# Kernel optimization log

Measured on AMD Instinct MI355X. Metric: run time of the kernel, lower is better.

Reference implementation:

```python
import jax, jax.numpy as jnp
import numpy as np

BS, N = 4, 4096
C_IN, C_DSSP, C_HID, NB = 384, 64, 128, 4


def setup_inputs() -> dict:
    key = jax.random.key(0)
    ks = jax.random.split(key, 12)
    sc = lambda k, sh, fan: jax.random.normal(k, sh, jnp.float32) / np.sqrt(fan)
    return {
        "s": jax.random.normal(ks[0], (BS, N, C_IN), jnp.float32),
        "s_initial": jax.random.normal(ks[1], (BS, N, C_IN), jnp.float32),
        "dssp": jax.random.normal(ks[2], (BS, N, C_DSSP), jnp.float32),
        "W_in": sc(ks[3], (C_HID, C_IN), C_IN), "b_in": jnp.zeros((C_HID,), jnp.float32),
        "W_init": sc(ks[4], (C_HID, C_IN), C_IN), "b_init": jnp.zeros((C_HID,), jnp.float32),
        "W_dssp": sc(ks[5], (C_HID, C_DSSP), C_DSSP), "b_dssp": jnp.zeros((C_HID,), jnp.float32),
        "W1": sc(ks[6], (NB, C_HID, C_HID), C_HID), "b1": jnp.zeros((NB, C_HID), jnp.float32),
        "W2": sc(ks[7], (NB, C_HID, C_HID), C_HID), "b2": jnp.zeros((NB, C_HID), jnp.float32),
        "W_out": sc(ks[8], (5, C_HID), C_HID), "b_out": jnp.zeros((5,), jnp.float32),
        "W_mult": sc(ks[9], (2, C_HID), C_HID), "b_mult": jnp.zeros((2,), jnp.float32),
        "scaling_modifier": jnp.float32(0.01),
    }


def reference(s, s_initial, dssp, W_in, b_in, W_init, b_init, W_dssp, b_dssp,
              W1, b1, W2, b2, W_out, b_out, W_mult, b_mult, scaling_modifier):
    relu = jax.nn.relu
    sp = jax.nn.softplus
    lin = lambda x, W, b: jnp.einsum('bnc,hc->bnh', x, W) + b

    h = lin(relu(s), W_in, b_in) + lin(relu(s_initial), W_init, b_init) + lin(relu(dssp), W_dssp, b_dssp)
    for i in range(W1.shape[0]):  # resnet blocks
        h = h + lin(relu(lin(relu(h), W1[i], b1[i])), W2[i], b2[i])
    hr = relu(h)
    corr = lin(hr, W_out, b_out)          # [bs, N, 5]
    mult = lin(hr, W_mult, b_mult)        # [bs, N, 2]
    a, bm = mult[..., 0], mult[..., 1]

    bs, n = corr.shape[0], corr.shape[1]
    idx = jnp.arange(n)
    # diagonal: set corr[...,0], then where(eye) -> sp(diag)*sp(a)+sp(b)
    d0 = sp(corr[..., 0]) * sp(a) + sp(bm)
    # subdiag -1: (i,i-1) += corr[:,i,1]  and  (i+1,i) += corr[:,i,3] (same cells)
    d1 = corr[:, 1:, 1] + corr[:, :-1, 3]
    # subdiag -2: (i,i-2) += corr[:,i,2]  and  (i+2,i) += corr[:,i,4]
    d2 = corr[:, 2:, 2] + corr[:, :-2, 4]

    L = jnp.zeros((bs, n, n), corr.dtype)
    L = L.at[:, idx, idx].set(d0)
    L = L.at[:, idx[1:], idx[:-1]].set(d1)
    L = L.at[:, idx[2:], idx[:-2]].set(d2)
    return scaling_modifier * L  # already lower-banded; tril is identity
```

## Files before the change

### kernel.cpp

```cpp
#include <hip/hip_runtime.h>
#include <math.h>

typedef __bf16 bf16_t;
typedef bf16_t bf16x8 __attribute__((ext_vector_type(8)));
typedef float  floatx4 __attribute__((ext_vector_type(4)));

constexpr int N_SEQ = 4096, BSZ = 4, CIN = 384, CDSSP = 64, CHID = 128, NBLK = 4;
constexpr int NTOK = BSZ * N_SEQ;
constexpr int TOK_PER_WAVE  = 32;
constexpr int MLP_BLOCKS  = NTOK / TOK_PER_WAVE;

constexpr int U_SIN   = 0;
constexpr int U_SINIT = 12288;
constexpr int U_DSSP  = 24576;
constexpr int U_W1    = 26624;
constexpr int U_W2    = 43008;
constexpr int U_END   = 59392;
constexpr int BAND_OFF = U_END * 4;

__device__ __forceinline__ float softplus_f(float x) {
    return fmaxf(x, 0.f) + log1pf(expf(-fabsf(x)));
}
__device__ __forceinline__ unsigned short bf16_bits(bf16_t h) {
    union { bf16_t b; unsigned short u; } c; c.b = h; return c.u;
}
__device__ __forceinline__ bf16_t bits_bf16(unsigned int u) {
    union { unsigned short u; bf16_t b; } c; c.u = (unsigned short)u; return c.b;
}
__device__ __forceinline__ floatx4 mfma16(bf16x8 a, bf16x8 b, floatx4 c) {
    return __builtin_amdgcn_mfma_f32_16x16x32_bf16(a, b, c, 0, 0, 0);
}

__global__ __launch_bounds__(256) void prep_weights(
    const float* __restrict__ Win, const float* __restrict__ Winit,
    const float* __restrict__ Wd,  const float* __restrict__ W1,
    const float* __restrict__ W2,  bf16_t* __restrict__ wsb)
{
    const int t = (int)blockIdx.x * 256 + (int)threadIdx.x;
    const float* src; int K, hi_base, plane, u;
    if (t < 6144)       { src = Win;   K = CIN;   hi_base = U_SIN;   plane = 6144; u = t; }
    else if (t < 12288) { src = Winit; K = CIN;   hi_base = U_SINIT; plane = 6144; u = t - 6144; }
    else if (t < 13312) { src = Wd;    K = CDSSP; hi_base = U_DSSP;  plane = 1024; u = t - 12288; }
    else if (t < 21504) { const int tt = t - 13312, rb = tt >> 11; u = tt & 2047;
                          src = W1 + (size_t)rb * CHID * CHID; K = CHID;
                          hi_base = U_W1 + rb * 4096; plane = 2048; }
    else                { const int tt = t - 21504, rb = tt >> 11; u = tt & 2047;
                          src = W2 + (size_t)rb * CHID * CHID; K = CHID;
                          hi_base = U_W2 + rb * 4096; plane = 2048; }
    const int K8 = K >> 3;
    const int nt = u / (16 * K8);
    const int r  = u - nt * 16 * K8;
    const int kg = r >> 6, r2 = r & 63, c = r2 >> 2, qq = r2 & 3;
    const int j = nt * 16 + c, k8 = kg * 4 + qq;
    const float* sp = src + (size_t)j * K + k8 * 8;
    const float4 a = *(const float4*)sp;
    const float4 b = *(const float4*)(sp + 4);
    const float xs[8] = { a.x, a.y, a.z, a.w, b.x, b.y, b.z, b.w };
    bf16x8 vh, vl;
    #pragma unroll
    for (int i = 0; i < 8; ++i) {
        const float x = xs[i];
        const bf16_t h = (bf16_t)x;
        vh[i] = h; vl[i] = (bf16_t)(x - (float)h);
    }
    *(bf16x8*)(wsb + ((size_t)hi_base + u) * 8)         = vh;
    *(bf16x8*)(wsb + ((size_t)hi_base + plane + u) * 8) = vl;
}

struct BF { bf16x8 h[8]; bf16x8 l[8]; };

__device__ __forceinline__ void loadB(const bf16_t* __restrict__ plane, int K8,
                                      int kg, int col, int q, BF& B) {
    const bf16_t* base = plane + (size_t)(kg * 64 + col * 4 + q) * 8;
    const size_t lo  = (size_t)128 * K8 * 8;
    const size_t nts = (size_t)16 * K8 * 8;
    #pragma unroll
    for (int nt = 0; nt < 8; ++nt) {
        B.h[nt] = *(const bf16x8*)(base + nt * nts);
        B.l[nt] = *(const bf16x8*)(base + nt * nts + lo);
    }
}

__device__ __forceinline__ void mfma_step(const bf16x8 (&ahi)[2], const bf16x8 (&alo)[2],
                                          const BF& B, floatx4 (&ac)[2][8]) {
    #pragma unroll
    for (int nt = 0; nt < 8; ++nt)
        #pragma unroll
        for (int mt = 0; mt < 2; ++mt) {
            ac[mt][nt] = mfma16(ahi[mt], B.h[nt], ac[mt][nt]);
            ac[mt][nt] = mfma16(alo[mt], B.h[nt], ac[mt][nt]);
            ac[mt][nt] = mfma16(ahi[mt], B.l[nt], ac[mt][nt]);
        }
}

__device__ __forceinline__ void packXA(const float4 (&X)[2][2],
                                       bf16x8 (&ahi)[2], bf16x8 (&alo)[2]) {
    #pragma unroll
    for (int mt = 0; mt < 2; ++mt) {
        const float xs[8] = { X[mt][0].x, X[mt][0].y, X[mt][0].z, X[mt][0].w,
                              X[mt][1].x, X[mt][1].y, X[mt][1].z, X[mt][1].w };
        #pragma unroll
        for (int i = 0; i < 8; ++i) {
            const float r = fmaxf(xs[i], 0.f);
            const bf16_t h = (bf16_t)r;
            ahi[mt][i] = h;
            alo[mt][i] = (bf16_t)(r - (float)h);
        }
    }
}

__device__ __forceinline__ void ldsA(const uint32_t (*A)[132], int kg, int col, int q,
                                     bf16x8 (&ahi)[2], bf16x8 (&alo)[2]) {
    #pragma unroll
    for (int mt = 0; mt < 2; ++mt) {
        const uint32_t* p = &A[mt * 16 + col][kg * 32 + q * 8];
        const uint4 u0 = *(const uint4*)p;
        const uint4 u1 = *(const uint4*)(p + 4);
        const uint32_t uu[8] = { u0.x, u0.y, u0.z, u0.w, u1.x, u1.y, u1.z, u1.w };
        union { uint32_t u[4]; bf16x8 v; } ch, cl;
        #pragma unroll
        for (int i = 0; i < 4; ++i) {
            ch.u[i] = (uu[2*i] & 0xffffu) | (uu[2*i+1] << 16);
            cl.u[i] = (uu[2*i] >> 16) | (uu[2*i+1] & 0xffff0000u);
        }
        ahi[mt] = ch.v; alo[mt] = cl.v;
    }
}

__device__ __forceinline__ void hidden_pass(const uint32_t (*A)[132],
    const bf16_t* __restrict__ plane, int col, int q, floatx4 (&ac)[2][8])
{
    BF B[2];
    loadB(plane, 16, 0, col, q, B[0]);
    #pragma unroll 1
    for (int kg = 0; kg < 4; kg += 2) {
        loadB(plane, 16, kg + 1, col, q, B[1]);
        bf16x8 ahi[2], alo[2];
        ldsA(A, kg, col, q, ahi, alo);
        mfma_step(ahi, alo, B[0], ac);
        if (kg + 2 < 4) loadB(plane, 16, kg + 2, col, q, B[0]);
        ldsA(A, kg + 1, col, q, ahi, alo);
        mfma_step(ahi, alo, B[1], ac);
    }
}

__global__ __launch_bounds__(64) void mlp_kernel(
    const float* __restrict__ s, const float* __restrict__ s_init,
    const float* __restrict__ dssp,
    const float* __restrict__ b_in, const float* __restrict__ b_init,
    const float* __restrict__ b_dssp,
    const float* __restrict__ b1, const float* __restrict__ b2,
    const float* __restrict__ W_out, const float* __restrict__ b_out,
    const float* __restrict__ W_mult, const float* __restrict__ b_mult,
    const bf16_t* __restrict__ wsb, float* __restrict__ band)
{
    __shared__ uint32_t A[32][132];

    const int lane = (int)threadIdx.x;
    const int col  = lane & 15;
    const int q    = lane >> 4;
    const int t0w  = (int)blockIdx.x * TOK_PER_WAVE;

    floatx4 hacc[2][8];
    #pragma unroll
    for (int nt = 0; nt < 8; ++nt) {
        const int j = nt * 16 + col;
        const float b = b_in[j] + b_init[j] + b_dssp[j];
        floatx4 v = { b, b, b, b };
        hacc[0][nt] = v; hacc[1][nt] = v;
    }

    auto loadA = [&](const float* __restrict__ src, int C, int kg, float4 (&X)[2][2]) {
        #pragma unroll
        for (int mt = 0; mt < 2; ++mt) {
            const float* p = src + (size_t)(t0w + mt * 16 + col) * C + kg * 32 + q * 8;
            X[mt][0] = *(const float4*)p;
            X[mt][1] = *(const float4*)(p + 4);
        }
    };

    #pragma unroll 1
    for (int seg = 0; seg < 3; ++seg) {
        const float* src = (seg == 0) ? s : (seg == 1) ? s_init : dssp;
        const int C   = (seg == 2) ? CDSSP : CIN;
        const int NKG = C >> 5;
        const int K8  = C >> 3;
        const bf16_t* plane = wsb +
            (size_t)((seg == 0) ? U_SIN : (seg == 1) ? U_SINIT : U_DSSP) * 8;

        float4 XA[2][2][2];
        BF B[2];
        loadA(src, C, 0, XA[0]);
        loadB(plane, K8, 0, col, q, B[0]);
        #pragma unroll 1
        for (int kg = 0; kg < NKG; kg += 2) {
            if (kg + 1 < NKG) { loadA(src, C, kg + 1, XA[1]); loadB(plane, K8, kg + 1, col, q, B[1]); }
            bf16x8 ahi[2], alo[2];
            packXA(XA[0], ahi, alo);
            mfma_step(ahi, alo, B[0], hacc);
            if (kg + 2 < NKG) { loadA(src, C, kg + 2, XA[0]); loadB(plane, K8, kg + 2, col, q, B[0]); }
            if (kg + 1 < NKG) {
                packXA(XA[1], ahi, alo);
                mfma_step(ahi, alo, B[1], hacc);
            }
        }
    }

    auto exchange = [&](floatx4 (&ac)[2][8]) {
        #pragma unroll
        for (int mt = 0; mt < 2; ++mt)
        #pragma unroll
        for (int nt = 0; nt < 8; ++nt)
        #pragma unroll
        for (int r = 0; r < 4; ++r) {
            const float x = fmaxf(ac[mt][nt][r], 0.f);
            const bf16_t h = (bf16_t)x;
            const bf16_t l = (bf16_t)(x - (float)h);
            A[mt * 16 + q * 4 + r][nt * 16 + col] =
                (uint32_t)bf16_bits(h) | ((uint32_t)bf16_bits(l) << 16);
        }
        __syncthreads();
    };

    #pragma unroll 1
    for (int rb = 0; rb < NBLK; ++rb) {
        exchange(hacc);
        floatx4 vacc[2][8];
        #pragma unroll
        for (int nt = 0; nt < 8; ++nt) {
            const float b = b1[rb * CHID + nt * 16 + col];
            floatx4 v = { b, b, b, b };
            vacc[0][nt] = v; vacc[1][nt] = v;
        }
        hidden_pass(A, wsb + ((size_t)U_W1 + rb * 4096) * 8, col, q, vacc);

        exchange(vacc);
        #pragma unroll
        for (int nt = 0; nt < 8; ++nt) {
            const float b = b2[rb * CHID + nt * 16 + col];
            #pragma unroll
            for (int mt = 0; mt < 2; ++mt) {
                floatx4 tt = hacc[mt][nt];
                tt[0] += b; tt[1] += b; tt[2] += b; tt[3] += b;
                hacc[mt][nt] = tt;
            }
        }
        hidden_pass(A, wsb + ((size_t)U_W2 + rb * 4096) * 8, col, q, hacc);
    }
    exchange(hacc);

    const int t    = lane & 31;
    const int half = lane >> 5;
    float d0v, d1v, d2v, d3v;
    const float *w0, *w1, *w2, *w3;
    if (half == 0) {
        w0 = W_out;          w1 = W_out + CHID; w2 = W_out + 2*CHID; w3 = W_out + 3*CHID;
        d0v = b_out[0]; d1v = b_out[1]; d2v = b_out[2]; d3v = b_out[3];
    } else {
        w0 = W_out + 4*CHID; w1 = W_mult;       w2 = W_mult + CHID;  w3 = W_out;
        d0v = b_out[4]; d1v = b_mult[0]; d2v = b_mult[1]; d3v = 0.f;
    }
    #pragma unroll 1
    for (int k = 0; k < CHID; ++k) {
        const uint32_t pk = A[t][k];
        const float x = (float)bits_bf16(pk & 0xffffu) + (float)bits_bf16(pk >> 16);
        d0v = fmaf(x, w0[k], d0v);
        d1v = fmaf(x, w1[k], d1v);
        d2v = fmaf(x, w2[k], d2v);
        d3v = fmaf(x, w3[k], d3v);
    }
    const float av = __shfl(d1v, 32 + t);
    const float bv = __shfl(d2v, 32 + t);
    const int g = t0w + t;
    if (half == 0) {
        band[g]            = softplus_f(d0v) * softplus_f(av) + softplus_f(bv);
        band[NTOK + g]     = d1v;
        band[2*NTOK + g]   = d2v;
        band[3*NTOK + g]   = d3v;
    } else {
        band[4*NTOK + g]   = d0v;
    }
}

__global__ __launch_bounds__(256) void zero_fill(float* __restrict__ out)
{
    floatx4* dst = (floatx4*)(out + (size_t)blockIdx.x * 32768);
    const floatx4 z = { 0.f, 0.f, 0.f, 0.f };
    #pragma unroll 1
    for (int i = (int)threadIdx.x; i < 8192; i += 256)
        __builtin_nontemporal_store(z, dst + i);
}

__global__ __launch_bounds__(256) void band_patch(
    const float* __restrict__ band, const float* __restrict__ p_sm,
    float* __restrict__ out)
{
    const int g = (int)blockIdx.x * 256 + (int)threadIdx.x;
    const int b = g >> 12;
    const int i = g & (N_SEQ - 1);
    const float sm = *p_sm;
    const size_t rowbase = (size_t)b * N_SEQ * N_SEQ + (size_t)i * N_SEQ;
    out[rowbase + i] = sm * band[g];
    if (i >= 1) out[rowbase + i - 1] = sm * (band[NTOK + g] + band[3*NTOK + g - 1]);
    if (i >= 2) out[rowbase + i - 2] = sm * (band[2*NTOK + g] + band[4*NTOK + g - 2]);
}

extern "C" void kernel_launch(void* const* d_in, const int* in_sizes, int n_in,
                              void* d_out, int out_size, void* d_ws, size_t ws_size,
                              hipStream_t stream)
{
    const float* s      = (const float*)d_in[0];
    const float* s_init = (const float*)d_in[1];
    const float* dssp   = (const float*)d_in[2];
    const float* W_in   = (const float*)d_in[3];
    const float* b_in   = (const float*)d_in[4];
    const float* W_init = (const float*)d_in[5];
    const float* b_initp= (const float*)d_in[6];
    const float* W_dssp = (const float*)d_in[7];
    const float* b_dsspp= (const float*)d_in[8];
    const float* W1     = (const float*)d_in[9];
    const float* b1     = (const float*)d_in[10];
    const float* W2     = (const float*)d_in[11];
    const float* b2     = (const float*)d_in[12];
    const float* W_out  = (const float*)d_in[13];
    const float* b_out  = (const float*)d_in[14];
    const float* W_mult = (const float*)d_in[15];
    const float* b_mult = (const float*)d_in[16];
    const float* sm     = (const float*)d_in[17];
    bf16_t* wsb  = (bf16_t*)d_ws;
    float*  band = (float*)d_ws + BAND_OFF;
    float*  out  = (float*)d_out;

    prep_weights<<<116, 256, 0, stream>>>(W_in, W_init, W_dssp, W1, W2, wsb);

    mlp_kernel<<<MLP_BLOCKS, 64, 0, stream>>>(
        s, s_init, dssp, b_in, b_initp, b_dsspp, b1, b2,
        W_out, b_out, W_mult, b_mult, (const bf16_t*)wsb, band);

    zero_fill<<<2048, 256, 0, stream>>>(out);

    band_patch<<<NTOK / 256, 256, 0, stream>>>(band, sm, out);
}
```

Before: 403.0 us.

## Pre-split activations into bf16 hi/lo workspace and fuse zero-fill into MLP launch

Activations are now ReLU'd and split into bf16 hi/lo planes in a prep kernel, stored in an MFMA-ready per-lane layout. The MLP input projection then streams these with coalesced loads instead of converting fp32 inline. Weights are re-laid out so each k-group chunk is contiguous per lane. The output zero-fill is merged into the MLP launch as extra blocks so it can overlap the MLP waves. The MFMA steps are reordered into three passes (hi·hi, lo·hi, hi·lo). The cost is an extra ~27 MB workspace write and read for the split activations.

```diff
diff --git a/kernel.cpp b/kernel.cpp
--- a/kernel.cpp
+++ b/kernel.cpp
@@ -9,14 +9,19 @@
 constexpr int NTOK = BSZ * N_SEQ;
 constexpr int TOK_PER_WAVE  = 32;
 constexpr int MLP_BLOCKS  = NTOK / TOK_PER_WAVE;
-
-constexpr int U_SIN   = 0;
-constexpr int U_SINIT = 12288;
-constexpr int U_DSSP  = 24576;
-constexpr int U_W1    = 26624;
-constexpr int U_W2    = 43008;
-constexpr int U_END   = 59392;
-constexpr int BAND_OFF = U_END * 4;
+constexpr int FILL_BLOCKS = 8192;
+constexpr size_t OUT_ELEMS = (size_t)BSZ * N_SEQ * N_SEQ;
+
+constexpr int U_BIN   = 0;
+constexpr int U_HID   = 26624;
+constexpr int B_END_U = 59392;
+constexpr int A_HI_U  = 59392;
+constexpr int A_UNITS = 1703936;
+constexpr int A_LO_U  = A_HI_U + A_UNITS;
+constexpr int WS_END_U = A_LO_U + A_UNITS;
+constexpr int BAND_OFF = WS_END_U * 4;
+constexpr int PREP_B_THREADS = 29696;
+constexpr int PREP_A_THREADS = A_UNITS;
 
 __device__ __forceinline__ float softplus_f(float x) {
     return fmaxf(x, 0.f) + log1pf(expf(-fabsf(x)));
@@ -31,53 +36,76 @@
     return __builtin_amdgcn_mfma_f32_16x16x32_bf16(a, b, c, 0, 0, 0);
 }
 
-__global__ __launch_bounds__(256) void prep_weights(
+__global__ __launch_bounds__(256) void prep_kernel(
+    const float* __restrict__ s, const float* __restrict__ s_init,
+    const float* __restrict__ dssp,
     const float* __restrict__ Win, const float* __restrict__ Winit,
     const float* __restrict__ Wd,  const float* __restrict__ W1,
     const float* __restrict__ W2,  bf16_t* __restrict__ wsb)
 {
-    const int t = (int)blockIdx.x * 256 + (int)threadIdx.x;
-    const float* src; int K, hi_base, plane, u;
-    if (t < 6144)       { src = Win;   K = CIN;   hi_base = U_SIN;   plane = 6144; u = t; }
-    else if (t < 12288) { src = Winit; K = CIN;   hi_base = U_SINIT; plane = 6144; u = t - 6144; }
-    else if (t < 13312) { src = Wd;    K = CDSSP; hi_base = U_DSSP;  plane = 1024; u = t - 12288; }
-    else if (t < 21504) { const int tt = t - 13312, rb = tt >> 11; u = tt & 2047;
-                          src = W1 + (size_t)rb * CHID * CHID; K = CHID;
-                          hi_base = U_W1 + rb * 4096; plane = 2048; }
-    else                { const int tt = t - 21504, rb = tt >> 11; u = tt & 2047;
-                          src = W2 + (size_t)rb * CHID * CHID; K = CHID;
-                          hi_base = U_W2 + rb * 4096; plane = 2048; }
-    const int K8 = K >> 3;
-    const int nt = u / (16 * K8);
-    const int r  = u - nt * 16 * K8;
-    const int kg = r >> 6, r2 = r & 63, c = r2 >> 2, qq = r2 & 3;
-    const int j = nt * 16 + c, k8 = kg * 4 + qq;
-    const float* sp = src + (size_t)j * K + k8 * 8;
-    const float4 a = *(const float4*)sp;
-    const float4 b = *(const float4*)(sp + 4);
-    const float xs[8] = { a.x, a.y, a.z, a.w, b.x, b.y, b.z, b.w };
-    bf16x8 vh, vl;
-    #pragma unroll
-    for (int i = 0; i < 8; ++i) {
-        const float x = xs[i];
-        const bf16_t h = (bf16_t)x;
-        vh[i] = h; vl[i] = (bf16_t)(x - (float)h);
-    }
-    *(bf16x8*)(wsb + ((size_t)hi_base + u) * 8)         = vh;
-    *(bf16x8*)(wsb + ((size_t)hi_base + plane + u) * 8) = vl;
+    const int g = (int)blockIdx.x * 256 + (int)threadIdx.x;
+    if (g < PREP_B_THREADS) {
+        const int c = g >> 9, r = g & 511;
+        const int nt = r >> 6, lane = r & 63, col = lane & 15, q = lane >> 4;
+        const int j = nt * 16 + col;
+        const float* W; int C, kgl, cu;
+        if (c < 12)      { W = Win;   C = CIN;   kgl = c;      cu = c; }
+        else if (c < 24) { W = Winit; C = CIN;   kgl = c - 12; cu = c; }
+        else if (c < 26) { W = Wd;    C = CDSSP; kgl = c - 24; cu = c; }
+        else {
+            const int hc = c - 26, m = hc >> 2;
+            W = (m & 1) ? W2 : W1;
+            W += (size_t)(m >> 1) * CHID * CHID;
+            C = CHID; kgl = hc & 3; cu = c;
+        }
+        const float* sp = W + (size_t)j * C + (kgl * 4 + q) * 8;
+        const float4 a = *(const float4*)sp;
+        const float4 b = *(const float4*)(sp + 4);
+        const float xs[8] = { a.x, a.y, a.z, a.w, b.x, b.y, b.z, b.w };
+        bf16x8 vh, vl;
+        #pragma unroll
+        for (int i = 0; i < 8; ++i) {
+            const float x = xs[i];
+            const bf16_t h = (bf16_t)x;
+            vh[i] = h; vl[i] = (bf16_t)(x - (float)h);
+        }
+        *(bf16x8*)(wsb + ((size_t)cu * 1024 + r) * 8)       = vh;
+        *(bf16x8*)(wsb + ((size_t)cu * 1024 + 512 + r) * 8) = vl;
+    } else {
+        const int t2 = g - PREP_B_THREADS;
+        const int w  = t2 / 3328;
+        const int r  = t2 - w * 3328;
+        const int kg = r >> 7, r2 = r & 127;
+        const int mt = r2 >> 6, lane = r2 & 63, col = lane & 15, q = lane >> 4;
+        const int token = w * 32 + mt * 16 + col;
+        const float* src; int C, kgl;
+        if (kg < 12)      { src = s;      C = CIN;   kgl = kg; }
+        else if (kg < 24) { src = s_init; C = CIN;   kgl = kg - 12; }
+        else              { src = dssp;   C = CDSSP; kgl = kg - 24; }
+        const float* sp = src + (size_t)token * C + kgl * 32 + q * 8;
+        const float4 a = *(const float4*)sp;
+        const float4 b = *(const float4*)(sp + 4);
+        const float xs[8] = { a.x, a.y, a.z, a.w, b.x, b.y, b.z, b.w };
+        bf16x8 vh, vl;
+        #pragma unroll
+        for (int i = 0; i < 8; ++i) {
+            const float x = fmaxf(xs[i], 0.f);
+            const bf16_t h = (bf16_t)x;
+            vh[i] = h; vl[i] = (bf16_t)(x - (float)h);
+        }
+        *(bf16x8*)(wsb + ((size_t)A_HI_U + t2) * 8) = vh;
+        *(bf16x8*)(wsb + ((size_t)A_LO_U + t2) * 8) = vl;
+    }
 }
 
 struct BF { bf16x8 h[8]; bf16x8 l[8]; };
 
-__device__ __forceinline__ void loadB(const bf16_t* __restrict__ plane, int K8,
-                                      int kg, int col, int q, BF& B) {
-    const bf16_t* base = plane + (size_t)(kg * 64 + col * 4 + q) * 8;
-    const size_t lo  = (size_t)128 * K8 * 8;
-    const size_t nts = (size_t)16 * K8 * 8;
+__device__ __forceinline__ void loadB(const bf16_t* __restrict__ img, int kg, int lane, BF& B) {
+    const bf16_t* cb = img + (size_t)(kg * 1024 + lane) * 8;
     #pragma unroll
     for (int nt = 0; nt < 8; ++nt) {
-        B.h[nt] = *(const bf16x8*)(base + nt * nts);
-        B.l[nt] = *(const bf16x8*)(base + nt * nts + lo);
+        B.h[nt] = *(const bf16x8*)(cb + (size_t)(nt * 64) * 8);
+        B.l[nt] = *(const bf16x8*)(cb + (size_t)(512 + nt * 64) * 8);
     }
 }
 
@@ -86,27 +114,18 @@
     #pragma unroll
     for (int nt = 0; nt < 8; ++nt)
         #pragma unroll
-        for (int mt = 0; mt < 2; ++mt) {
+        for (int mt = 0; mt < 2; ++mt)
             ac[mt][nt] = mfma16(ahi[mt], B.h[nt], ac[mt][nt]);
+    #pragma unroll
+    for (int nt = 0; nt < 8; ++nt)
+        #pragma unroll
+        for (int mt = 0; mt < 2; ++mt)
             ac[mt][nt] = mfma16(alo[mt], B.h[nt], ac[mt][nt]);
+    #pragma unroll
+    for (int nt = 0; nt < 8; ++nt)
+        #pragma unroll
+        for (int mt = 0; mt < 2; ++mt)
             ac[mt][nt] = mfma16(ahi[mt], B.l[nt], ac[mt][nt]);
-        }
-}
-
-__device__ __forceinline__ void packXA(const float4 (&X)[2][2],
-                                       bf16x8 (&ahi)[2], bf16x8 (&alo)[2]) {
-    #pragma unroll
-    for (int mt = 0; mt < 2; ++mt) {
-        const float xs[8] = { X[mt][0].x, X[mt][0].y, X[mt][0].z, X[mt][0].w,
-                              X[mt][1].x, X[mt][1].y, X[mt][1].z, X[mt][1].w };
-        #pragma unroll
-        for (int i = 0; i < 8; ++i) {
-            const float r = fmaxf(xs[i], 0.f);
-            const bf16_t h = (bf16_t)r;
-            ahi[mt][i] = h;
-            alo[mt][i] = (bf16_t)(r - (float)h);
-        }
-    }
 }
 
 __device__ __forceinline__ void ldsA(const uint32_t (*A)[132], int kg, int col, int q,
@@ -128,38 +147,45 @@
 }
 
 __device__ __forceinline__ void hidden_pass(const uint32_t (*A)[132],
-    const bf16_t* __restrict__ plane, int col, int q, floatx4 (&ac)[2][8])
+    const bf16_t* __restrict__ img, int lane, int col, int q, floatx4 (&ac)[2][8])
 {
     BF B[2];
-    loadB(plane, 16, 0, col, q, B[0]);
+    loadB(img, 0, lane, B[0]);
     #pragma unroll 1
-    for (int kg = 0; kg < 4; kg += 2) {
-        loadB(plane, 16, kg + 1, col, q, B[1]);
+    for (int kg = 0; kg < 4; ++kg) {
+        if (kg < 3) loadB(img, kg + 1, lane, B[(kg + 1) & 1]);
         bf16x8 ahi[2], alo[2];
         ldsA(A, kg, col, q, ahi, alo);
-        mfma_step(ahi, alo, B[0], ac);
-        if (kg + 2 < 4) loadB(plane, 16, kg + 2, col, q, B[0]);
-        ldsA(A, kg + 1, col, q, ahi, alo);
-        mfma_step(ahi, alo, B[1], ac);
-    }
-}
-
-__global__ __launch_bounds__(64) void mlp_kernel(
-    const float* __restrict__ s, const float* __restrict__ s_init,
-    const float* __restrict__ dssp,
+        mfma_step(ahi, alo, B[kg & 1], ac);
+    }
+}
+
+__global__ __launch_bounds__(64) void mlp_fill_kernel(
     const float* __restrict__ b_in, const float* __restrict__ b_init,
     const float* __restrict__ b_dssp,
     const float* __restrict__ b1, const float* __restrict__ b2,
     const float* __restrict__ W_out, const float* __restrict__ b_out,
     const float* __restrict__ W_mult, const float* __restrict__ b_mult,
-    const bf16_t* __restrict__ wsb, float* __restrict__ band)
+    const bf16_t* __restrict__ wsb, float* __restrict__ band,
+    float* __restrict__ out)
 {
     __shared__ uint32_t A[32][132];
+
+    if (blockIdx.x >= MLP_BLOCKS) {
+        const int f = (int)blockIdx.x - MLP_BLOCKS;
+        floatx4* dst = (floatx4*)out + (size_t)f * 2048;
+        const floatx4 z = { 0.f, 0.f, 0.f, 0.f };
+        #pragma unroll 1
+        for (int i = (int)threadIdx.x; i < 2048; i += 64)
+            __builtin_nontemporal_store(z, dst + i);
+        return;
+    }
 
     const int lane = (int)threadIdx.x;
     const int col  = lane & 15;
     const int q    = lane >> 4;
-    const int t0w  = (int)blockIdx.x * TOK_PER_WAVE;
+    const int w    = (int)blockIdx.x;
+    const int t0w  = w * TOK_PER_WAVE;
 
     floatx4 hacc[2][8];
     #pragma unroll
@@ -170,39 +196,28 @@
         hacc[0][nt] = v; hacc[1][nt] = v;
     }
 
-    auto loadA = [&](const float* __restrict__ src, int C, int kg, float4 (&X)[2][2]) {
-        #pragma unroll
-        for (int mt = 0; mt < 2; ++mt) {
-            const float* p = src + (size_t)(t0w + mt * 16 + col) * C + kg * 32 + q * 8;
-            X[mt][0] = *(const float4*)p;
-            X[mt][1] = *(const float4*)(p + 4);
-        }
-    };
-
-    #pragma unroll 1
-    for (int seg = 0; seg < 3; ++seg) {
-        const float* src = (seg == 0) ? s : (seg == 1) ? s_init : dssp;
-        const int C   = (seg == 2) ? CDSSP : CIN;
-        const int NKG = C >> 5;
-        const int K8  = C >> 3;
-        const bf16_t* plane = wsb +
-            (size_t)((seg == 0) ? U_SIN : (seg == 1) ? U_SINIT : U_DSSP) * 8;
-
-        float4 XA[2][2][2];
+    {
+        const bf16_t* ab = wsb + ((size_t)A_HI_U + (size_t)w * 3328 + lane) * 8;
+        auto loadA = [&](int kg, bf16x8 (&ahi)[2], bf16x8 (&alo)[2]) {
+            const bf16_t* p = ab + (size_t)(kg * 128) * 8;
+            #pragma unroll
+            for (int mt = 0; mt < 2; ++mt) {
+                ahi[mt] = *(const bf16x8*)(p + (size_t)(mt * 64) * 8);
+                alo[mt] = *(const bf16x8*)(p + ((size_t)A_UNITS + mt * 64) * 8);
+            }
+        };
         BF B[2];
-        loadA(src, C, 0, XA[0]);
-        loadB(plane, K8, 0, col, q, B[0]);
+        bf16x8 AH[2][2], AL[2][2];
+        loadA(0, AH[0], AL[0]);
+        loadB(wsb, 0, lane, B[0]);
         #pragma unroll 1
-        for (int kg = 0; kg < NKG; kg += 2) {
-            if (kg + 1 < NKG) { loadA(src, C, kg + 1, XA[1]); loadB(plane, K8, kg + 1, col, q, B[1]); }
-            bf16x8 ahi[2], alo[2];
-            packXA(XA[0], ahi, alo);
-            mfma_step(ahi, alo, B[0], hacc);
-            if (kg + 2 < NKG) { loadA(src, C, kg + 2, XA[0]); loadB(plane, K8, kg + 2, col, q, B[0]); }
-            if (kg + 1 < NKG) {
-                packXA(XA[1], ahi, alo);
-                mfma_step(ahi, alo, B[1], hacc);
+        for (int kg = 0; kg < 26; ++kg) {
+            const int cur = kg & 1, nxt = cur ^ 1;
+            if (kg + 1 < 26) {
+                loadA(kg + 1, AH[nxt], AL[nxt]);
+                loadB(wsb, kg + 1, lane, B[nxt]);
             }
+            mfma_step(AH[cur], AL[cur], B[cur], hacc);
         }
     }
 
@@ -232,7 +247,7 @@
             floatx4 v = { b, b, b, b };
             vacc[0][nt] = v; vacc[1][nt] = v;
         }
-        hidden_pass(A, wsb + ((size_t)U_W1 + rb * 4096) * 8, col, q, vacc);
+        hidden_pass(A, wsb + (size_t)(U_HID + (rb * 2 + 0) * 4096) * 8, lane, col, q, vacc);
 
         exchange(vacc);
         #pragma unroll
@@ -245,7 +260,7 @@
                 hacc[mt][nt] = tt;
             }
         }
-        hidden_pass(A, wsb + ((size_t)U_W2 + rb * 4096) * 8, col, q, hacc);
+        hidden_pass(A, wsb + (size_t)(U_HID + (rb * 2 + 1) * 4096) * 8, lane, col, q, hacc);
     }
     exchange(hacc);
 
@@ -280,15 +295,6 @@
     } else {
         band[4*NTOK + g]   = d0v;
     }
-}
-
-__global__ __launch_bounds__(256) void zero_fill(float* __restrict__ out)
-{
-    floatx4* dst = (floatx4*)(out + (size_t)blockIdx.x * 32768);
-    const floatx4 z = { 0.f, 0.f, 0.f, 0.f };
-    #pragma unroll 1
-    for (int i = (int)threadIdx.x; i < 8192; i += 256)
-        __builtin_nontemporal_store(z, dst + i);
 }
 
 __global__ __launch_bounds__(256) void band_patch(
@@ -331,13 +337,13 @@
     float*  band = (float*)d_ws + BAND_OFF;
     float*  out  = (float*)d_out;
 
-    prep_weights<<<116, 256, 0, stream>>>(W_in, W_init, W_dssp, W1, W2, wsb);
-
-    mlp_kernel<<<MLP_BLOCKS, 64, 0, stream>>>(
-        s, s_init, dssp, b_in, b_initp, b_dsspp, b1, b2,
-        W_out, b_out, W_mult, b_mult, (const bf16_t*)wsb, band);
-
-    zero_fill<<<2048, 256, 0, stream>>>(out);
+    const int prep_blocks = (PREP_B_THREADS + PREP_A_THREADS) / 256;
+    prep_kernel<<<prep_blocks, 256, 0, stream>>>(
+        s, s_init, dssp, W_in, W_init, W_dssp, W1, W2, wsb);
+
+    mlp_fill_kernel<<<MLP_BLOCKS + FILL_BLOCKS, 64, 0, stream>>>(
+        b_in, b_initp, b_dsspp, b1, b2,
+        W_out, b_out, W_mult, b_mult, (const bf16_t*)wsb, band, out);
 
     band_patch<<<NTOK / 256, 256, 0, stream>>>(band, sm, out);
 }
```

After: 669.5 us. 1.66x slower.
